# Performance work log

Measured on AMD Instinct MI355X. Metric: run time of the kernel, lower is better.

Reference implementation:

```python
import jax, jax.numpy as jnp
import numpy as np

MAT_DIM = 4  # quaternion algebra vector size
EMBED_DIM = 1024
NUM_HEADS = 16
HEAD_DIM = EMBED_DIM // NUM_HEADS  # 64
SCALE = 1.0 / np.sqrt(HEAD_DIM)


def quaternion_structure():
    # C[i,j,k]: e_i * e_j = sum_k C[i,j,k] e_k, basis (1, i, j, k)
    C = np.zeros((4, 4, 4), dtype=np.float32)
    table = [
        (0, 0, 0, 1.0), (0, 1, 1, 1.0), (0, 2, 2, 1.0), (0, 3, 3, 1.0),
        (1, 0, 1, 1.0), (2, 0, 2, 1.0), (3, 0, 3, 1.0),
        (1, 1, 0, -1.0), (2, 2, 0, -1.0), (3, 3, 0, -1.0),
        (1, 2, 3, 1.0), (2, 1, 3, -1.0),
        (2, 3, 1, 1.0), (3, 2, 1, -1.0),
        (3, 1, 2, 1.0), (1, 3, 2, -1.0),
    ]
    for i, j, k, s in table:
        C[i, j, k] = s
    return jnp.asarray(C)


def algebra_linear(x, W, b, C):
    # x: [B,S,Nin,d] algebra-blocked input; W: [Nout,Nin,d]; b: [Nout,d]
    # y[b,s,o,k] = sum_{n,i,j} C[i,j,k] W[o,n,i] x[b,s,n,j] + b[o,k]
    Wm = jnp.einsum('oni,ijk->onjk', W, C)  # left-multiplication matrices
    return jnp.einsum('bsnj,onjk->bsok', x, Wm) + b


def setup_inputs() -> dict:
    key = jax.random.key(0)
    ks = jax.random.split(key, 6)
    B, S = 2, 2048
    nb = EMBED_DIM // MAT_DIM  # 256 algebra blocks
    w_std = 0.02
    inp = {
        'x': jax.random.normal(ks[0], (B, S, EMBED_DIM), dtype=jnp.float32),
        'mask': jnp.ones((1, 1, S, S), dtype=jnp.int32),
        'Wq': jax.random.normal(ks[1], (nb, nb, MAT_DIM), dtype=jnp.float32) * w_std,
        'bq': jnp.zeros((nb, MAT_DIM), dtype=jnp.float32),
        'Wk': jax.random.normal(ks[2], (nb, nb, MAT_DIM), dtype=jnp.float32) * w_std,
        'bk': jnp.zeros((nb, MAT_DIM), dtype=jnp.float32),
        'Wv': jax.random.normal(ks[3], (nb, nb, MAT_DIM), dtype=jnp.float32) * w_std,
        'bv': jnp.zeros((nb, MAT_DIM), dtype=jnp.float32),
        'Wo': jax.random.normal(ks[4], (nb, nb, MAT_DIM), dtype=jnp.float32) * w_std,
        'bo': jnp.zeros((nb, MAT_DIM), dtype=jnp.float32),
    }
    return inp


def reference(x, mask, Wq, bq, Wk, bk, Wv, bv, Wo, bo):
    C = quaternion_structure()
    B, S, E = x.shape
    xb = x.reshape(B, S, E // MAT_DIM, MAT_DIM)

    q = algebra_linear(xb, Wq, bq, C).reshape(B, S, E)
    k = algebra_linear(xb, Wk, bk, C).reshape(B, S, E)
    v = algebra_linear(xb, Wv, bv, C).reshape(B, S, E)

    def split_heads(t):  # [B,S,E] -> [B,H,S,hd]
        return t.reshape(B, S, NUM_HEADS, HEAD_DIM).transpose(0, 2, 1, 3)

    q, k, v = split_heads(q), split_heads(k), split_heads(v)

    scores = jnp.einsum('bhqd,bhkd->bhqk', q, k) * SCALE
    scores = jnp.where(mask == 0, -jnp.inf, scores)
    attn = jax.nn.softmax(scores, axis=-1)
    context = jnp.einsum('bhqk,bhkd->bhqd', attn, v)
    context = context.transpose(0, 2, 1, 3).reshape(B, S, E)

    cb = context.reshape(B, S, E // MAT_DIM, MAT_DIM)
    out = algebra_linear(cb, Wo, bo, C).reshape(B, S, E)
    return out
```

## Files before the change

kernel.cpp:

```cpp
#include <hip/hip_runtime.h>
#include <hip/hip_bf16.h>

typedef __attribute__((ext_vector_type(8))) short bf16x8;
typedef __attribute__((ext_vector_type(4))) float f32x4;
typedef __attribute__((ext_vector_type(16))) float f32x16;
typedef __attribute__((ext_vector_type(4))) unsigned short u16x4;
typedef __attribute__((ext_vector_type(4))) unsigned int u32x4;
typedef __attribute__((ext_vector_type(2))) unsigned int u32x2;

#define LOG2E 1.4426950408889634f
#define SCLOG 0.18033688011118312f
#define EXP2(x) __builtin_amdgcn_exp2f(x)

static __device__ __forceinline__ unsigned short f2bf(float f) {
  __hip_bfloat16 h = __float2bfloat16(f);
  return __builtin_bit_cast(unsigned short, h);
}
static __device__ __forceinline__ float bf2f(unsigned short u) {
  __hip_bfloat16 h = __builtin_bit_cast(__hip_bfloat16, u);
  return __bfloat162float(h);
}
static __device__ __forceinline__ unsigned cvtpk(float lo, float hg) {
  unsigned r;
  asm("v_cvt_pk_bf16_f32 %0, %1, %2" : "=v"(r) : "v"(lo), "v"(hg));
  return r;
}
static __device__ __forceinline__ bf16x8 ld16(const void* p) {
  return *(const bf16x8*)p;
}
static __device__ __forceinline__ void gload16(const void* g, void* l) {
  __builtin_amdgcn_global_load_lds(
      (const __attribute__((address_space(1))) void*)g,
      (__attribute__((address_space(3))) void*)l, 16, 0, 0);
}

__global__ void prep(const float* __restrict__ x,
                     const int* __restrict__ mask,
                     const float* __restrict__ Wq,
                     const float* __restrict__ Wk,
                     const float* __restrict__ Wv,
                     const float* __restrict__ Wo,
                     unsigned short* __restrict__ xb,
                     unsigned short* __restrict__ Mqkv,
                     unsigned short* __restrict__ Mo,
                     unsigned long long* __restrict__ bits_t)
{
  const int bx = blockIdx.x, tid = threadIdx.x;
  if (bx < 16384) {
    const int g = bx * 256 + tid;
    const unsigned long long w = __ballot(mask[g] != 0);
    if ((tid & 63) == 0) {
      const int idx = g >> 6;
      const int sq = idx >> 5, kw = idx & 31;
      bits_t[(size_t)kw * 2048 + sq] = w;
    }
  } else if (bx < 20480) {
    const int i = (bx - 16384) * 256 + tid;
    const float4 a = ((const float4*)x)[i];
    u32x2 o; o[0] = cvtpk(a.x, a.y); o[1] = cvtpk(a.z, a.w);
    ((u32x2*)xb)[i] = o;
  } else {
    const int e = bx - 20480;
    const int mat = e >> 8;
    const int o = e & 255;
    const int n = tid;
    const float* W = (mat == 0) ? Wq : (mat == 1) ? Wk : (mat == 2) ? Wv : Wo;
    unsigned short* M = (mat < 3) ? (Mqkv + (size_t)mat * 1024 * 1024) : Mo;
    const float4 w = *(const float4*)(W + ((size_t)o * 256 + n) * 4);
    const unsigned short w0 = f2bf(w.x), w1 = f2bf(w.y), w2 = f2bf(w.z), w3 = f2bf(w.w);
#define NG(u) ((unsigned short)((u) ^ 0x8000))
    u16x4 r0; r0[0] = w0;     r0[1] = NG(w1); r0[2] = NG(w2); r0[3] = NG(w3);
    u16x4 r1; r1[0] = w1;     r1[1] = w0;     r1[2] = NG(w3); r1[3] = w2;
    u16x4 r2; r2[0] = w2;     r2[1] = w3;     r2[2] = w0;     r2[3] = NG(w1);
    u16x4 r3; r3[0] = w3;     r3[1] = NG(w2); r3[2] = w1;     r3[3] = w0;
#undef NG
    unsigned short* dst = M + (size_t)(o * 4) * 1024 + n * 4;
    *(u16x4*)(dst)        = r0;
    *(u16x4*)(dst + 1024) = r1;
    *(u16x4*)(dst + 2048) = r2;
    *(u16x4*)(dst + 3072) = r3;
  }
}

template <int MODE, int BM>
__global__ __launch_bounds__(256, 3)
void gemm_bt(const unsigned short* __restrict__ A,
             const unsigned short* __restrict__ Bm,
             const float* __restrict__ bias0,
             const float* __restrict__ bias1,
             const float* __restrict__ bias2,
             unsigned short* __restrict__ out0,
             unsigned short* __restrict__ out1,
             unsigned short* __restrict__ out2,
             float* __restrict__ fout)
{
  constexpr int K = 1024;
  constexpr int FR = BM / 32;
  __shared__ unsigned short As[BM * 64];
  __shared__ unsigned short Bs[128 * 64];
  const int tid = threadIdx.x;
  const int lane = tid & 63;
  const int wave = tid >> 6;
  const int bn = blockIdx.x, bm = blockIdx.y;
  const int wm = wave >> 1, wn = wave & 1;
  const int l15 = lane & 15, l4 = lane >> 4;

  f32x4 zero4 = {0.f, 0.f, 0.f, 0.f};
  f32x4 acc[FR][4];
#pragma unroll
  for (int i = 0; i < FR; ++i)
#pragma unroll
    for (int j = 0; j < 4; ++j) acc[i][j] = zero4;

  for (int kk = 0; kk < K; kk += 64) {
#pragma unroll
    for (int c = 0; c < BM / 32; ++c) {
      const int Lb = (wave * (BM / 32) + c) * 1024;
      const int L = Lb + lane * 16;
      const int row = L >> 7;
      const int slot = (L >> 4) & 7;
      const int ss = slot ^ (row & 7);
      gload16(A + (size_t)(bm * BM + row) * K + kk + ss * 8, (char*)As + Lb);
    }
#pragma unroll
    for (int c = 0; c < 4; ++c) {
      const int Lb = (wave * 4 + c) * 1024;
      const int L = Lb + lane * 16;
      const int row = L >> 7;
      const int slot = (L >> 4) & 7;
      const int ss = slot ^ (row & 7);
      gload16(Bm + (size_t)(bn * 128 + row) * K + kk + ss * 8, (char*)Bs + Lb);
    }
    __syncthreads();
#pragma unroll
    for (int ks = 0; ks < 2; ++ks) {
      bf16x8 af[FR], bfr[4];
#pragma unroll
      for (int i = 0; i < FR; ++i) {
        const int ra = wm * (BM / 2) + i * 16 + l15;
        const int sa = (ks * 4 + l4) ^ (ra & 7);
        af[i] = ld16((const char*)As + ra * 128 + sa * 16);
      }
#pragma unroll
      for (int j = 0; j < 4; ++j) {
        const int rb = wn * 64 + j * 16 + l15;
        const int sb = (ks * 4 + l4) ^ (rb & 7);
        bfr[j] = ld16((const char*)Bs + rb * 128 + sb * 16);
      }
#pragma unroll
      for (int i = 0; i < FR; ++i)
#pragma unroll
        for (int j = 0; j < 4; ++j)
          acc[i][j] = __builtin_amdgcn_mfma_f32_16x16x32_bf16(af[i], bfr[j], acc[i][j], 0, 0, 0);
    }
    __syncthreads();
  }

#pragma unroll
  for (int i = 0; i < FR; ++i) {
    const int t0 = bm * BM + wm * (BM / 2) + i * 16 + l4 * 4;
#pragma unroll
    for (int j = 0; j < 4; ++j) {
      const int e = bn * 128 + wn * 64 + j * 16 + l15;
      f32x4 v = acc[i][j];
      if (MODE == 0) {
        const int which = e >> 10;
        const int e1 = e & 1023;
        const float* bp = (which == 0) ? bias0 : (which == 1 ? bias1 : bias2);
        const float bias = bp[e1];
        if (which == 0) {
#pragma unroll
          for (int r = 0; r < 4; ++r)
            out0[(size_t)(t0 + r) * 1024 + e1] = f2bf((v[r] + bias) * SCLOG);
        } else if (which == 1) {
#pragma unroll
          for (int r = 0; r < 4; ++r)
            out1[(size_t)(t0 + r) * 1024 + e1] = f2bf(v[r] + bias);
        } else {
          const int h = e1 >> 6, d = e1 & 63;
          const int b = t0 >> 11, s = t0 & 2047;
          u16x4 pk;
#pragma unroll
          for (int r = 0; r < 4; ++r) pk[r] = f2bf(v[r] + bias);
          *(u16x4*)&out2[((size_t)((b * 16 + h) * 64 + d)) * 2048 + s] = pk;
        }
      } else {
        const float bias = bias0[e];
#pragma unroll
        for (int r = 0; r < 4; ++r)
          fout[(size_t)(t0 + r) * 1024 + e] = v[r] + bias;
      }
    }
  }
}

__global__ __launch_bounds__(256, 4)
void attn_fwd(const unsigned short* __restrict__ q,
              const unsigned short* __restrict__ k,
              const unsigned short* __restrict__ vt,
              const unsigned long long* __restrict__ mbt,
              unsigned short* __restrict__ po,
              float* __restrict__ sbuf)
{
  constexpr int S = 2048;
  __shared__ __align__(16) unsigned short Ks[2 * 4096];
  __shared__ __align__(16) unsigned short Vs[2 * 4096];

  const int bid = blockIdx.x;
  const int vb = (bid & 7) * 128 + (bid >> 3);
  const int half = vb & 1;
  const int qg = (vb >> 1) & 15;
  const int bh = vb >> 5;
  const int b = bh >> 4, h = bh & 15;

  const int tid = threadIdx.x, lane = tid & 63, wave = tid >> 6;
  const int l31 = lane & 31, hif = lane >> 5;
  const int sq = qg * 128 + wave * 32 + l31;
  const size_t gq = (size_t)b * S + sq;

  bf16x8 bqf[4];
#pragma unroll
  for (int s = 0; s < 4; ++s)
    bqf[s] = ld16(q + gq * 1024 + h * 64 + s * 16 + hif * 8);

  f32x16 o0 = {}, o1 = {};
  float la0 = 0.f, la1 = 0.f;
  const int k0 = half * 16;

#define STAGE(bufi, kti)                                                                  \
  {                                                                                       \
    _Pragma("unroll")                                                                     \
    for (int c = 0; c < 2; ++c) {                                                         \
      const int sl = c * 256 + tid;                                                       \
      const int row = sl >> 3;                                                            \
      const int ss = (sl & 7) ^ (row & 7);                                                \
      gload16(k + (size_t)(b * S + (kti) * 64 + row) * 1024 + h * 64 + ss * 8,            \
              (char*)Ks + (bufi) * 8192 + (c * 4 + wave) * 1024);                         \
      gload16(vt + (size_t)(bh * 64 + row) * 2048 + (kti) * 64 + ss * 8,                  \
              (char*)Vs + (bufi) * 8192 + (c * 4 + wave) * 1024);                         \
    }                                                                                     \
  }

  STAGE(0, k0);
  __syncthreads();

  int buf = 0;
  for (int kt = k0; kt < k0 + 16; ++kt) {
    const unsigned long long w = mbt[(size_t)kt * 2048 + sq];
    if (kt + 1 < k0 + 16) STAGE(buf ^ 1, kt + 1);

    const char* Kb = (const char*)Ks + buf * 8192;
    const char* Vb = (const char*)Vs + buf * 8192;

#pragma unroll
    for (int sub = 0; sub < 2; ++sub) {
      f32x16 p = {};
      const int kr = sub * 32 + l31;
      __builtin_amdgcn_s_setprio(1);
#pragma unroll
      for (int s = 0; s < 4; ++s) {
        const int slot = s * 2 + hif;
        bf16x8 a0 = ld16(Kb + kr * 128 + ((slot ^ (kr & 7)) << 4));
        p = __builtin_amdgcn_mfma_f32_32x32x16_bf16(a0, bqf[s], p, 0, 0, 0);
      }
      __builtin_amdgcn_s_setprio(0);

      const unsigned wsub = (unsigned)(w >> (sub * 32));
      if (!__all(wsub == 0xffffffffu)) {
#pragma unroll
        for (int c = 0; c < 16; ++c) {
          const int key = (c & 3) + 8 * (c >> 2) + 4 * hif;
          if (!((wsub >> key) & 1u)) p[c] = -INFINITY;
        }
      }

#pragma unroll
      for (int c = 0; c < 16; ++c) p[c] = EXP2(p[c]);

      float sm[8];
#pragma unroll
      for (int c = 0; c < 8; ++c) sm[c] = p[c] + p[c + 8];
#pragma unroll
      for (int d = 4; d; d >>= 1)
#pragma unroll
        for (int c = 0; c < d; ++c) sm[c] += sm[c + d];
      const float ts = sm[0] + __shfl_xor(sm[0], 32, 64);
      if (sub == 0) la0 += ts; else la1 += ts;

      u32x4 bpw[2];
#pragma unroll
      for (int ks = 0; ks < 2; ++ks) {
        const int rb2 = ks * 8;
        unsigned X0 = cvtpk(p[rb2 + 0], p[rb2 + 1]);
        unsigned X1 = cvtpk(p[rb2 + 2], p[rb2 + 3]);
        unsigned Y0 = cvtpk(p[rb2 + 4], p[rb2 + 5]);
        unsigned Y1 = cvtpk(p[rb2 + 6], p[rb2 + 7]);
        asm("v_permlane32_swap_b32 %0, %1" : "+v"(X0), "+v"(Y0));
        asm("v_permlane32_swap_b32 %0, %1" : "+v"(X1), "+v"(Y1));
        bpw[ks][0] = X0;
        bpw[ks][1] = X1;
        bpw[ks][2] = Y0;
        bpw[ks][3] = Y1;
      }

      __builtin_amdgcn_s_setprio(1);
#pragma unroll
      for (int ks = 0; ks < 2; ++ks) {
        const bf16x8 bfrag = __builtin_bit_cast(bf16x8, bpw[ks]);
        const int slot = (sub * 2 + ks) * 2 + hif;
        const int r0 = l31, r1 = 32 + l31;
        bf16x8 v0 = ld16(Vb + r0 * 128 + ((slot ^ (r0 & 7)) << 4));
        bf16x8 v1 = ld16(Vb + r1 * 128 + ((slot ^ (r1 & 7)) << 4));
        o0 = __builtin_amdgcn_mfma_f32_32x32x16_bf16(v0, bfrag, o0, 0, 0, 0);
        o1 = __builtin_amdgcn_mfma_f32_32x32x16_bf16(v1, bfrag, o1, 0, 0, 0);
      }
      __builtin_amdgcn_s_setprio(0);
    }

    __syncthreads();
    buf ^= 1;
  }
#undef STAGE

  const float l = la0 + la1;
  const float inv = (l > 0.f) ? 1.f / l : 0.f;
  const float s = (l > 0.f) ? __log2f(l) : -1e30f;
  unsigned short* cp = po + ((size_t)(half * 32 + bh) * 2048 + sq) * 64;
#pragma unroll
  for (int g = 0; g < 4; ++g) {
    u32x2 s0, s1;
    s0[0] = cvtpk(o0[g * 4 + 0] * inv, o0[g * 4 + 1] * inv);
    s0[1] = cvtpk(o0[g * 4 + 2] * inv, o0[g * 4 + 3] * inv);
    s1[0] = cvtpk(o1[g * 4 + 0] * inv, o1[g * 4 + 1] * inv);
    s1[1] = cvtpk(o1[g * 4 + 2] * inv, o1[g * 4 + 3] * inv);
    *(u32x2*)(cp + g * 8 + hif * 4) = s0;
    *(u32x2*)(cp + 32 + g * 8 + hif * 4) = s1;
  }
  if (hif == 0) sbuf[half * 65536 + bh * 2048 + sq] = s;
}

__global__ void merge_halves(const unsigned short* __restrict__ po,
                             const float* __restrict__ sbuf,
                             unsigned short* __restrict__ ctx)
{
  const int t = blockIdx.x * 256 + threadIdx.x;
  const int row = t >> 3;
  const int d0 = (t & 7) * 8;
  const int bh = row >> 11, sq = row & 2047;
  const int b = bh >> 4, h = bh & 15;

  const float s0 = sbuf[row];
  const float s1 = sbuf[65536 + row];
  const bf16x8 a = ld16(po + (size_t)row * 64 + d0);
  const bf16x8 c = ld16(po + 4194304 + (size_t)row * 64 + d0);
  const float smax = fmaxf(s0, s1);
  float w0 = EXP2(s0 - smax), w1 = EXP2(s1 - smax);
  const float winv = 1.f / (w0 + w1);
  w0 *= winv; w1 *= winv;

  float f[8];
#pragma unroll
  for (int j = 0; j < 8; ++j)
    f[j] = w0 * bf2f((unsigned short)a[j]) + w1 * bf2f((unsigned short)c[j]);
  u32x4 r;
  r[0] = cvtpk(f[0], f[1]);
  r[1] = cvtpk(f[2], f[3]);
  r[2] = cvtpk(f[4], f[5]);
  r[3] = cvtpk(f[6], f[7]);
  *(u32x4*)(ctx + ((size_t)b * 2048 + sq) * 1024 + h * 64 + d0) = r;
}

extern "C" void kernel_launch(void* const* d_in, const int* in_sizes, int n_in,
                              void* d_out, int out_size, void* d_ws, size_t ws_size,
                              hipStream_t stream)
{
  const float* x  = (const float*)d_in[0];
  const int* mask = (const int*)d_in[1];
  const float* Wq = (const float*)d_in[2];
  const float* bq = (const float*)d_in[3];
  const float* Wk = (const float*)d_in[4];
  const float* bk = (const float*)d_in[5];
  const float* Wv = (const float*)d_in[6];
  const float* bv = (const float*)d_in[7];
  const float* Wo = (const float*)d_in[8];
  const float* bo = (const float*)d_in[9];

  char* ws = (char*)d_ws;
  unsigned short* Mqkv = (unsigned short*)(ws);
  unsigned short* Mo   = (unsigned short*)(ws + (6ull  << 20));
  unsigned short* xb   = (unsigned short*)(ws + (8ull  << 20));
  unsigned short* ctx  = (unsigned short*)(ws + (8ull  << 20));
  unsigned short* qb_  = (unsigned short*)(ws + (16ull << 20));
  unsigned short* kb_  = (unsigned short*)(ws + (24ull << 20));
  unsigned short* vtb  = (unsigned short*)(ws + (32ull << 20));
  unsigned long long* bits = (unsigned long long*)(ws + (40ull << 20));
  float* sbuf = (float*)(ws + (40ull << 20) + (512ull << 10));
  unsigned short* po = (unsigned short*)d_out;

  prep<<<dim3(21504), 256, 0, stream>>>(x, mask, Wq, Wk, Wv, Wo, xb, Mqkv, Mo, bits);
  gemm_bt<0, 128><<<dim3(24, 32), 256, 0, stream>>>(xb, Mqkv, bq, bk, bv, qb_, kb_, vtb, nullptr);
  attn_fwd<<<dim3(1024), 256, 0, stream>>>(qb_, kb_, vtb, bits, po, sbuf);
  merge_halves<<<dim3(2048), 256, 0, stream>>>(po, sbuf, ctx);
  gemm_bt<1, 64><<<dim3(8, 64), 256, 0, stream>>>(ctx, Mo, bo, bo, bo, nullptr, nullptr, nullptr,
                                                  (float*)d_out);
}
```

Before: 113.5 us.

## Process two query tiles per wave in attention to reuse K/V LDS loads

```diff
diff --git a/kernel.cpp b/kernel.cpp
--- a/kernel.cpp
+++ b/kernel.cpp
@@ -194,7 +194,7 @@
   }
 }
 
-__global__ __launch_bounds__(256, 4)
+__global__ __launch_bounds__(256, 2)
 void attn_fwd(const unsigned short* __restrict__ q,
               const unsigned short* __restrict__ k,
               const unsigned short* __restrict__ vt,
@@ -207,24 +207,28 @@
   __shared__ __align__(16) unsigned short Vs[2 * 4096];
 
   const int bid = blockIdx.x;
-  const int vb = (bid & 7) * 128 + (bid >> 3);
+  const int vb = (bid & 7) * 64 + (bid >> 3);
   const int half = vb & 1;
-  const int qg = (vb >> 1) & 15;
-  const int bh = vb >> 5;
+  const int qg = (vb >> 1) & 7;
+  const int bh = vb >> 4;
   const int b = bh >> 4, h = bh & 15;
 
   const int tid = threadIdx.x, lane = tid & 63, wave = tid >> 6;
   const int l31 = lane & 31, hif = lane >> 5;
-  const int sq = qg * 128 + wave * 32 + l31;
-  const size_t gq = (size_t)b * S + sq;
-
-  bf16x8 bqf[4];
-#pragma unroll
-  for (int s = 0; s < 4; ++s)
-    bqf[s] = ld16(q + gq * 1024 + h * 64 + s * 16 + hif * 8);
-
-  f32x16 o0 = {}, o1 = {};
-  float la0 = 0.f, la1 = 0.f;
+  const int sq0 = qg * 256 + wave * 64 + l31;
+  const int sq1 = sq0 + 32;
+  const size_t gq0 = (size_t)b * S + sq0;
+  const size_t gq1 = (size_t)b * S + sq1;
+
+  bf16x8 bqfA[4], bqfB[4];
+#pragma unroll
+  for (int s = 0; s < 4; ++s) {
+    bqfA[s] = ld16(q + gq0 * 1024 + h * 64 + s * 16 + hif * 8);
+    bqfB[s] = ld16(q + gq1 * 1024 + h * 64 + s * 16 + hif * 8);
+  }
+
+  f32x16 o00 = {}, o01 = {}, o10 = {}, o11 = {};
+  float lA = 0.f, lB = 0.f;
   const int k0 = half * 16;
 
 #define STAGE(bufi, kti)                                                                  \
@@ -246,7 +250,8 @@
 
   int buf = 0;
   for (int kt = k0; kt < k0 + 16; ++kt) {
-    const unsigned long long w = mbt[(size_t)kt * 2048 + sq];
+    const unsigned long long w0 = mbt[(size_t)kt * 2048 + sq0];
+    const unsigned long long w1 = mbt[(size_t)kt * 2048 + sq1];
     if (kt + 1 < k0 + 16) STAGE(buf ^ 1, kt + 1);
 
     const char* Kb = (const char*)Ks + buf * 8192;
@@ -254,65 +259,78 @@
 
 #pragma unroll
     for (int sub = 0; sub < 2; ++sub) {
-      f32x16 p = {};
       const int kr = sub * 32 + l31;
+      bf16x8 ak[4];
+#pragma unroll
+      for (int s = 0; s < 4; ++s)
+        ak[s] = ld16(Kb + kr * 128 + (((s * 2 + hif) ^ (kr & 7)) << 4));
+
+      f32x16 pA = {}, pB = {};
       __builtin_amdgcn_s_setprio(1);
 #pragma unroll
       for (int s = 0; s < 4; ++s) {
-        const int slot = s * 2 + hif;
-        bf16x8 a0 = ld16(Kb + kr * 128 + ((slot ^ (kr & 7)) << 4));
-        p = __builtin_amdgcn_mfma_f32_32x32x16_bf16(a0, bqf[s], p, 0, 0, 0);
+        pA = __builtin_amdgcn_mfma_f32_32x32x16_bf16(ak[s], bqfA[s], pA, 0, 0, 0);
+        pB = __builtin_amdgcn_mfma_f32_32x32x16_bf16(ak[s], bqfB[s], pB, 0, 0, 0);
       }
       __builtin_amdgcn_s_setprio(0);
 
-      const unsigned wsub = (unsigned)(w >> (sub * 32));
-      if (!__all(wsub == 0xffffffffu)) {
+      const unsigned wA = (unsigned)(w0 >> (sub * 32));
+      const unsigned wB = (unsigned)(w1 >> (sub * 32));
+      if (!__all((wA & wB) == 0xffffffffu)) {
 #pragma unroll
         for (int c = 0; c < 16; ++c) {
           const int key = (c & 3) + 8 * (c >> 2) + 4 * hif;
-          if (!((wsub >> key) & 1u)) p[c] = -INFINITY;
+          if (!((wA >> key) & 1u)) pA[c] = -INFINITY;
+          if (!((wB >> key) & 1u)) pB[c] = -INFINITY;
         }
       }
 
 #pragma unroll
-      for (int c = 0; c < 16; ++c) p[c] = EXP2(p[c]);
-
-      float sm[8];
-#pragma unroll
-      for (int c = 0; c < 8; ++c) sm[c] = p[c] + p[c + 8];
+      for (int c = 0; c < 16; ++c) { pA[c] = EXP2(pA[c]); pB[c] = EXP2(pB[c]); }
+
+      float smA[8], smB[8];
+#pragma unroll
+      for (int c = 0; c < 8; ++c) { smA[c] = pA[c] + pA[c + 8]; smB[c] = pB[c] + pB[c + 8]; }
 #pragma unroll
       for (int d = 4; d; d >>= 1)
 #pragma unroll
-        for (int c = 0; c < d; ++c) sm[c] += sm[c + d];
-      const float ts = sm[0] + __shfl_xor(sm[0], 32, 64);
-      if (sub == 0) la0 += ts; else la1 += ts;
-
-      u32x4 bpw[2];
+        for (int c = 0; c < d; ++c) { smA[c] += smA[c + d]; smB[c] += smB[c + d]; }
+      lA += smA[0] + __shfl_xor(smA[0], 32, 64);
+      lB += smB[0] + __shfl_xor(smB[0], 32, 64);
+
+      u32x4 bpwA[2], bpwB[2];
 #pragma unroll
       for (int ks = 0; ks < 2; ++ks) {
         const int rb2 = ks * 8;
-        unsigned X0 = cvtpk(p[rb2 + 0], p[rb2 + 1]);
-        unsigned X1 = cvtpk(p[rb2 + 2], p[rb2 + 3]);
-        unsigned Y0 = cvtpk(p[rb2 + 4], p[rb2 + 5]);
-        unsigned Y1 = cvtpk(p[rb2 + 6], p[rb2 + 7]);
-        asm("v_permlane32_swap_b32 %0, %1" : "+v"(X0), "+v"(Y0));
-        asm("v_permlane32_swap_b32 %0, %1" : "+v"(X1), "+v"(Y1));
-        bpw[ks][0] = X0;
-        bpw[ks][1] = X1;
-        bpw[ks][2] = Y0;
-        bpw[ks][3] = Y1;
+        unsigned XA0 = cvtpk(pA[rb2 + 0], pA[rb2 + 1]);
+        unsigned XA1 = cvtpk(pA[rb2 + 2], pA[rb2 + 3]);
+        unsigned YA0 = cvtpk(pA[rb2 + 4], pA[rb2 + 5]);
+        unsigned YA1 = cvtpk(pA[rb2 + 6], pA[rb2 + 7]);
+        asm("v_permlane32_swap_b32 %0, %1" : "+v"(XA0), "+v"(YA0));
+        asm("v_permlane32_swap_b32 %0, %1" : "+v"(XA1), "+v"(YA1));
+        bpwA[ks][0] = XA0; bpwA[ks][1] = XA1; bpwA[ks][2] = YA0; bpwA[ks][3] = YA1;
+        unsigned XB0 = cvtpk(pB[rb2 + 0], pB[rb2 + 1]);
+        unsigned XB1 = cvtpk(pB[rb2 + 2], pB[rb2 + 3]);
+        unsigned YB0 = cvtpk(pB[rb2 + 4], pB[rb2 + 5]);
+        unsigned YB1 = cvtpk(pB[rb2 + 6], pB[rb2 + 7]);
+        asm("v_permlane32_swap_b32 %0, %1" : "+v"(XB0), "+v"(YB0));
+        asm("v_permlane32_swap_b32 %0, %1" : "+v"(XB1), "+v"(YB1));
+        bpwB[ks][0] = XB0; bpwB[ks][1] = XB1; bpwB[ks][2] = YB0; bpwB[ks][3] = YB1;
       }
 
       __builtin_amdgcn_s_setprio(1);
 #pragma unroll
       for (int ks = 0; ks < 2; ++ks) {
-        const bf16x8 bfrag = __builtin_bit_cast(bf16x8, bpw[ks]);
         const int slot = (sub * 2 + ks) * 2 + hif;
         const int r0 = l31, r1 = 32 + l31;
         bf16x8 v0 = ld16(Vb + r0 * 128 + ((slot ^ (r0 & 7)) << 4));
         bf16x8 v1 = ld16(Vb + r1 * 128 + ((slot ^ (r1 & 7)) << 4));
-        o0 = __builtin_amdgcn_mfma_f32_32x32x16_bf16(v0, bfrag, o0, 0, 0, 0);
-        o1 = __builtin_amdgcn_mfma_f32_32x32x16_bf16(v1, bfrag, o1, 0, 0, 0);
+        const bf16x8 fA = __builtin_bit_cast(bf16x8, bpwA[ks]);
+        const bf16x8 fB = __builtin_bit_cast(bf16x8, bpwB[ks]);
+        o00 = __builtin_amdgcn_mfma_f32_32x32x16_bf16(v0, fA, o00, 0, 0, 0);
+        o01 = __builtin_amdgcn_mfma_f32_32x32x16_bf16(v1, fA, o01, 0, 0, 0);
+        o10 = __builtin_amdgcn_mfma_f32_32x32x16_bf16(v0, fB, o10, 0, 0, 0);
+        o11 = __builtin_amdgcn_mfma_f32_32x32x16_bf16(v1, fB, o11, 0, 0, 0);
       }
       __builtin_amdgcn_s_setprio(0);
     }
@@ -322,21 +340,32 @@
   }
 #undef STAGE
 
-  const float l = la0 + la1;
-  const float inv = (l > 0.f) ? 1.f / l : 0.f;
-  const float s = (l > 0.f) ? __log2f(l) : -1e30f;
-  unsigned short* cp = po + ((size_t)(half * 32 + bh) * 2048 + sq) * 64;
+  const float invA = (lA > 0.f) ? 1.f / lA : 0.f;
+  const float invB = (lB > 0.f) ? 1.f / lB : 0.f;
+  const float sA = (lA > 0.f) ? __log2f(lA) : -1e30f;
+  const float sB = (lB > 0.f) ? __log2f(lB) : -1e30f;
+  unsigned short* cpA = po + ((size_t)(half * 32 + bh) * 2048 + sq0) * 64;
+  unsigned short* cpB = po + ((size_t)(half * 32 + bh) * 2048 + sq1) * 64;
 #pragma unroll
   for (int g = 0; g < 4; ++g) {
-    u32x2 s0, s1;
-    s0[0] = cvtpk(o0[g * 4 + 0] * inv, o0[g * 4 + 1] * inv);
-    s0[1] = cvtpk(o0[g * 4 + 2] * inv, o0[g * 4 + 3] * inv);
-    s1[0] = cvtpk(o1[g * 4 + 0] * inv, o1[g * 4 + 1] * inv);
-    s1[1] = cvtpk(o1[g * 4 + 2] * inv, o1[g * 4 + 3] * inv);
-    *(u32x2*)(cp + g * 8 + hif * 4) = s0;
-    *(u32x2*)(cp + 32 + g * 8 + hif * 4) = s1;
-  }
-  if (hif == 0) sbuf[half * 65536 + bh * 2048 + sq] = s;
+    u32x2 a0, a1, b0, b1;
+    a0[0] = cvtpk(o00[g * 4 + 0] * invA, o00[g * 4 + 1] * invA);
+    a0[1] = cvtpk(o00[g * 4 + 2] * invA, o00[g * 4 + 3] * invA);
+    a1[0] = cvtpk(o01[g * 4 + 0] * invA, o01[g * 4 + 1] * invA);
+    a1[1] = cvtpk(o01[g * 4 + 2] * invA, o01[g * 4 + 3] * invA);
+    b0[0] = cvtpk(o10[g * 4 + 0] * invB, o10[g * 4 + 1] * invB);
+    b0[1] = cvtpk(o10[g * 4 + 2] * invB, o10[g * 4 + 3] * invB);
+    b1[0] = cvtpk(o11[g * 4 + 0] * invB, o11[g * 4 + 1] * invB);
+    b1[1] = cvtpk(o11[g * 4 + 2] * invB, o11[g * 4 + 3] * invB);
+    *(u32x2*)(cpA + g * 8 + hif * 4) = a0;
+    *(u32x2*)(cpA + 32 + g * 8 + hif * 4) = a1;
+    *(u32x2*)(cpB + g * 8 + hif * 4) = b0;
+    *(u32x2*)(cpB + 32 + g * 8 + hif * 4) = b1;
+  }
+  if (hif == 0) {
+    sbuf[half * 65536 + bh * 2048 + sq0] = sA;
+    sbuf[half * 65536 + bh * 2048 + sq1] = sB;
+  }
 }
 
 __global__ void merge_halves(const unsigned short* __restrict__ po,
@@ -399,7 +428,7 @@
 
   prep<<<dim3(21504), 256, 0, stream>>>(x, mask, Wq, Wk, Wv, Wo, xb, Mqkv, Mo, bits);
   gemm_bt<0, 128><<<dim3(24, 32), 256, 0, stream>>>(xb, Mqkv, bq, bk, bv, qb_, kb_, vtb, nullptr);
-  attn_fwd<<<dim3(1024), 256, 0, stream>>>(qb_, kb_, vtb, bits, po, sbuf);
+  attn_fwd<<<dim3(512), 256, 0, stream>>>(qb_, kb_, vtb, bits, po, sbuf);
   merge_halves<<<dim3(2048), 256, 0, stream>>>(po, sbuf, ctx);
   gemm_bt<1, 64><<<dim3(8, 64), 256, 0, stream>>>(ctx, Mo, bo, bo, bo, nullptr, nullptr, nullptr,
                                                   (float*)d_out);
```

Result: no change. 112.2 us (-1.1%).
